# Optimization experiments

Measured on AMD Instinct MI355X. Metric: run time of the kernel, lower is better.

Reference implementation:

```python
import jax, jax.numpy as jnp
import numpy as np


def setup_inputs() -> dict:
    key = jax.random.key(0)
    k1, k2 = jax.random.split(key)
    B, C, H, W = 16, 8, 512, 512
    pred = jax.random.normal(k1, (B, C, H, W), dtype=jnp.float32)
    target = jax.random.randint(k2, (B, H, W), 0, C, dtype=jnp.int64)
    return {"pred": pred, "target": target}


def reference(pred, target):
    # pred: (B,C,H,W) float; target: (B,H,W) int64. reduction='mean', no weights.
    B, C, H, W = pred.shape

    # ---- J loss (vectorized over all (ci,ck) class pairs) ----
    t1h = jax.nn.one_hot(target, C, axis=1, dtype=pred.dtype)   # (B,C,H,W)
    n_i = t1h.sum(axis=(2, 3))                                   # (B,C) per-class pixel counts
    phi = t1h / n_i[:, :, None, None]                            # (B,C,H,W)
    # M[b,ci,ck] = sum_hw pred[b,ci]*phi[b,ck]
    M = jnp.einsum('bchw,bkhw->bck', pred, phi)
    diag = jnp.diagonal(M, axis1=1, axis2=2)                     # (B,C) = sum pred_ci*phi_ci
    # delta_ik contraction: sum pred_ci*(phi_ci - phi_ck)/2
    inner = (diag[:, :, None] - M) * 0.5                         # (B,C,C), zero on diagonal
    w = jnp.ones((C, C), dtype=pred.dtype)                       # default j_wgt
    off_diag = 1.0 - jnp.eye(C, dtype=pred.dtype)
    loss = w[None] * jnp.log(0.5 + inner) * off_diag[None]       # (B,C,C)
    j = -loss.sum(axis=(1, 2))                                   # (B,)
    jl = j.mean()

    # ---- cross entropy on collapsed dims: logits (B,C,N), target (B,N) ----
    logits = pred.reshape(B, C, H * W)
    logp = jax.nn.log_softmax(logits, axis=1)
    tgt = target.reshape(B, H * W)
    nll = -jnp.take_along_axis(logp, tgt[:, None, :], axis=1)[:, 0, :]  # (B,N)
    ce = nll.mean()

    return jl + ce
```

## Files before the change

### kernel.cpp

```cpp
#include <hip/hip_runtime.h>

#define NB 16
#define NC 8
#define HW (512 * 512)
#define BLOCKS_PER_B 32
#define NTHREADS 256

#define WS_FLOATS (NB * NC * NC + NB * NC + 1)

__device__ __forceinline__ float wave_reduce(float v) {
#pragma unroll
  for (int off = 32; off > 0; off >>= 1) v += __shfl_xor(v, off, 64);
  return v;
}

__global__ __launch_bounds__(NTHREADS, 2)
void jce_main(const float* __restrict__ pred, const int* __restrict__ target,
              float* __restrict__ ws) {
  const int b = blockIdx.y;
  const int tid = threadIdx.x;
  const float* predb = pred + (size_t)b * NC * HW;
  const int4* tgt4 = (const int4*)(target + (size_t)b * HW);

  float S[NC][NC];
  float cnt[NC];
  float ce = 0.0f;
#pragma unroll
  for (int i = 0; i < NC; ++i) {
    cnt[i] = 0.0f;
#pragma unroll
    for (int k = 0; k < NC; ++k) S[i][k] = 0.0f;
  }

  const int ng = HW / 4;
#pragma unroll 2
  for (int g = blockIdx.x * NTHREADS + tid; g < ng; g += BLOCKS_PER_B * NTHREADS) {
    const int4 t4 = tgt4[g];
    float4 p4[NC];
#pragma unroll
    for (int c = 0; c < NC; ++c)
      p4[c] = ((const float4*)(predb + (size_t)c * HW))[g];

#pragma unroll
    for (int j = 0; j < 4; ++j) {
      const int tc = (j == 0) ? t4.x : (j == 1) ? t4.y : (j == 2) ? t4.z : t4.w;
      float pv[NC];
#pragma unroll
      for (int c = 0; c < NC; ++c)
        pv[c] = (j == 0) ? p4[c].x : (j == 1) ? p4[c].y : (j == 2) ? p4[c].z : p4[c].w;

      float es = 0.0f;
#pragma unroll
      for (int c = 0; c < NC; ++c) es += __expf(pv[c]);
      const float lse = __logf(es);

      float ptc = 0.0f;
#pragma unroll
      for (int k = 0; k < NC; ++k) {
        const float msk = (tc == k) ? 1.0f : 0.0f;
        cnt[k] += msk;
        ptc = fmaf(msk, pv[k], ptc);
#pragma unroll
        for (int ci = 0; ci < NC; ++ci)
          S[ci][k] = fmaf(msk, pv[ci], S[ci][k]);
      }
      ce += lse - ptc;
    }
  }

#pragma unroll
  for (int i = 0; i < NC; ++i) {
#pragma unroll
    for (int k = 0; k < NC; ++k) S[i][k] = wave_reduce(S[i][k]);
    cnt[i] = wave_reduce(cnt[i]);
  }
  ce = wave_reduce(ce);

  __shared__ float red[NTHREADS / 64][NC * NC + NC + 1];
  const int wave = tid >> 6, lane = tid & 63;
  if (lane == 0) {
#pragma unroll
    for (int i = 0; i < NC; ++i) {
#pragma unroll
      for (int k = 0; k < NC; ++k) red[wave][i * NC + k] = S[i][k];
      red[wave][NC * NC + i] = cnt[i];
    }
    red[wave][NC * NC + NC] = ce;
  }
  __syncthreads();
  if (tid < NC * NC + NC + 1) {
    float v = 0.0f;
#pragma unroll
    for (int w = 0; w < NTHREADS / 64; ++w) v += red[w][tid];
    if (tid < NC * NC)
      atomicAdd(&ws[b * (NC * NC) + tid], v);
    else if (tid < NC * NC + NC)
      atomicAdd(&ws[NB * NC * NC + b * NC + (tid - NC * NC)], v);
    else
      atomicAdd(&ws[NB * NC * NC + NB * NC], v);
  }
}

__global__ __launch_bounds__(NTHREADS)
void jce_finalize(const float* __restrict__ ws, float* __restrict__ out) {
  const int tid = threadIdx.x;
  float acc = 0.0f;
  for (int idx = tid; idx < NB * NC * NC; idx += NTHREADS) {
    const int b = idx >> 6, ci = (idx >> 3) & 7, ck = idx & 7;
    if (ci == ck) continue;
    const float n_ck = ws[NB * NC * NC + b * NC + ck];
    const float n_ci = ws[NB * NC * NC + b * NC + ci];
    const float M = ws[b * (NC * NC) + ci * NC + ck] / n_ck;
    const float dg = ws[b * (NC * NC) + ci * NC + ci] / n_ci;
    acc += logf(0.5f + 0.5f * (dg - M));
  }
  acc = wave_reduce(acc);
  __shared__ float red[NTHREADS / 64];
  const int wave = tid >> 6, lane = tid & 63;
  if (lane == 0) red[wave] = acc;
  __syncthreads();
  if (tid == 0) {
    float tot = 0.0f;
#pragma unroll
    for (int w = 0; w < NTHREADS / 64; ++w) tot += red[w];
    const float jl = -tot / (float)NB;
    const float ce = ws[NB * NC * NC + NB * NC] / ((float)NB * (float)HW);
    out[0] = jl + ce;
  }
}

extern "C" void kernel_launch(void* const* d_in, const int* in_sizes, int n_in,
                              void* d_out, int out_size, void* d_ws, size_t ws_size,
                              hipStream_t stream) {
  const float* pred = (const float*)d_in[0];
  const int* target = (const int*)d_in[1];
  float* out = (float*)d_out;
  float* ws = (float*)d_ws;

  hipMemsetAsync(ws, 0, WS_FLOATS * sizeof(float), stream);
  dim3 grid(BLOCKS_PER_B, NB);
  jce_main<<<grid, NTHREADS, 0, stream>>>(pred, target, ws);
  jce_finalize<<<1, NTHREADS, 0, stream>>>(ws, out);
}
```

Baseline: 212.4 us.

## Software-pipeline loads with double buffers and fuse finalize via last-block counter

```diff
diff --git a/kernel.cpp b/kernel.cpp
--- a/kernel.cpp
+++ b/kernel.cpp
@@ -5,8 +5,11 @@
 #define HW (512 * 512)
 #define BLOCKS_PER_B 32
 #define NTHREADS 256
+#define NBLOCKS (BLOCKS_PER_B * NB)
+#define STRIDE (BLOCKS_PER_B * NTHREADS)
 
-#define WS_FLOATS (NB * NC * NC + NB * NC + 1)
+#define WS_FLOATS (NB * NC * NC + NB * NC + 2)
+#define CTR_IDX (NB * NC * NC + NB * NC + 1)
 
 __device__ __forceinline__ float wave_reduce(float v) {
 #pragma unroll
@@ -16,11 +19,12 @@
 
 __global__ __launch_bounds__(NTHREADS, 2)
 void jce_main(const float* __restrict__ pred, const int* __restrict__ target,
-              float* __restrict__ ws) {
+              float* __restrict__ ws, float* __restrict__ out) {
   const int b = blockIdx.y;
   const int tid = threadIdx.x;
   const float* predb = pred + (size_t)b * NC * HW;
   const int4* tgt4 = (const int4*)(target + (size_t)b * HW);
+  const int g0 = blockIdx.x * NTHREADS + tid;
 
   float S[NC][NC];
   float cnt[NC];
@@ -32,41 +36,50 @@
     for (int k = 0; k < NC; ++k) S[i][k] = 0.0f;
   }
 
-  const int ng = HW / 4;
-#pragma unroll 2
-  for (int g = blockIdx.x * NTHREADS + tid; g < ng; g += BLOCKS_PER_B * NTHREADS) {
-    const int4 t4 = tgt4[g];
-    float4 p4[NC];
+  int4 tA, tB;
+  float4 pA[NC], pB[NC];
+
+#define LOAD(T, P, s)                                                      \
+  do {                                                                     \
+    const int gg = g0 + (s) * STRIDE;                                      \
+    T = tgt4[gg];                                                          \
+    _Pragma("unroll") for (int c = 0; c < NC; ++c)                         \
+        P[c] = ((const float4*)(predb + (size_t)c * HW))[gg];              \
+  } while (0)
+
+#define COMPUTE(T, P)                                                      \
+  do {                                                                     \
+    _Pragma("unroll") for (int j = 0; j < 4; ++j) {                        \
+      const int tc = (j == 0) ? T.x : (j == 1) ? T.y : (j == 2) ? T.z : T.w; \
+      float pv[NC];                                                        \
+      _Pragma("unroll") for (int c = 0; c < NC; ++c)                       \
+          pv[c] = (j == 0) ? P[c].x : (j == 1) ? P[c].y                    \
+                  : (j == 2) ? P[c].z : P[c].w;                            \
+      float es = 0.0f;                                                     \
+      _Pragma("unroll") for (int c = 0; c < NC; ++c) es += __expf(pv[c]);  \
+      const float lse = __logf(es);                                        \
+      float ptc = 0.0f;                                                    \
+      _Pragma("unroll") for (int k = 0; k < NC; ++k) {                     \
+        const float msk = (tc == k) ? 1.0f : 0.0f;                         \
+        cnt[k] += msk;                                                     \
+        ptc = fmaf(msk, pv[k], ptc);                                       \
+        _Pragma("unroll") for (int ci = 0; ci < NC; ++ci)                  \
+            S[ci][k] = fmaf(msk, pv[ci], S[ci][k]);                        \
+      }                                                                    \
+      ce += lse - ptc;                                                     \
+    }                                                                      \
+  } while (0)
+
+  LOAD(tA, pA, 0);
 #pragma unroll
-    for (int c = 0; c < NC; ++c)
-      p4[c] = ((const float4*)(predb + (size_t)c * HW))[g];
-
-#pragma unroll
-    for (int j = 0; j < 4; ++j) {
-      const int tc = (j == 0) ? t4.x : (j == 1) ? t4.y : (j == 2) ? t4.z : t4.w;
-      float pv[NC];
-#pragma unroll
-      for (int c = 0; c < NC; ++c)
-        pv[c] = (j == 0) ? p4[c].x : (j == 1) ? p4[c].y : (j == 2) ? p4[c].z : p4[c].w;
-
-      float es = 0.0f;
-#pragma unroll
-      for (int c = 0; c < NC; ++c) es += __expf(pv[c]);
-      const float lse = __logf(es);
-
-      float ptc = 0.0f;
-#pragma unroll
-      for (int k = 0; k < NC; ++k) {
-        const float msk = (tc == k) ? 1.0f : 0.0f;
-        cnt[k] += msk;
-        ptc = fmaf(msk, pv[k], ptc);
-#pragma unroll
-        for (int ci = 0; ci < NC; ++ci)
-          S[ci][k] = fmaf(msk, pv[ci], S[ci][k]);
-      }
-      ce += lse - ptc;
-    }
+  for (int s = 0; s < 8; s += 2) {
+    if (s + 1 < 8) LOAD(tB, pB, s + 1);
+    COMPUTE(tA, pA);
+    if (s + 2 < 8) LOAD(tA, pA, s + 2);
+    if (s + 1 < 8) COMPUTE(tB, pB);
   }
+#undef LOAD
+#undef COMPUTE
 
 #pragma unroll
   for (int i = 0; i < NC; ++i) {
@@ -99,33 +112,38 @@
     else
       atomicAdd(&ws[NB * NC * NC + NB * NC], v);
   }
-}
 
-__global__ __launch_bounds__(NTHREADS)
-void jce_finalize(const float* __restrict__ ws, float* __restrict__ out) {
-  const int tid = threadIdx.x;
+  __shared__ int is_last;
+  __syncthreads();
+  if (tid == 0) {
+    __threadfence();
+    unsigned prev = atomicAdd((unsigned*)&ws[CTR_IDX], 1u);
+    is_last = (prev == (unsigned)(NBLOCKS - 1)) ? 1 : 0;
+  }
+  __syncthreads();
+  if (!is_last) return;
+
   float acc = 0.0f;
   for (int idx = tid; idx < NB * NC * NC; idx += NTHREADS) {
-    const int b = idx >> 6, ci = (idx >> 3) & 7, ck = idx & 7;
+    const int bb = idx >> 6, ci = (idx >> 3) & 7, ck = idx & 7;
     if (ci == ck) continue;
-    const float n_ck = ws[NB * NC * NC + b * NC + ck];
-    const float n_ci = ws[NB * NC * NC + b * NC + ci];
-    const float M = ws[b * (NC * NC) + ci * NC + ck] / n_ck;
-    const float dg = ws[b * (NC * NC) + ci * NC + ci] / n_ci;
-    acc += logf(0.5f + 0.5f * (dg - M));
+    const float n_ck = atomicAdd(&ws[NB * NC * NC + bb * NC + ck], 0.0f);
+    const float n_ci = atomicAdd(&ws[NB * NC * NC + bb * NC + ci], 0.0f);
+    const float Sik = atomicAdd(&ws[bb * (NC * NC) + ci * NC + ck], 0.0f);
+    const float Sii = atomicAdd(&ws[bb * (NC * NC) + ci * NC + ci], 0.0f);
+    acc += logf(0.5f + 0.5f * (Sii / n_ci - Sik / n_ck));
   }
   acc = wave_reduce(acc);
-  __shared__ float red[NTHREADS / 64];
-  const int wave = tid >> 6, lane = tid & 63;
-  if (lane == 0) red[wave] = acc;
+  __shared__ float red2[NTHREADS / 64];
+  if (lane == 0) red2[wave] = acc;
   __syncthreads();
   if (tid == 0) {
     float tot = 0.0f;
 #pragma unroll
-    for (int w = 0; w < NTHREADS / 64; ++w) tot += red[w];
+    for (int w = 0; w < NTHREADS / 64; ++w) tot += red2[w];
     const float jl = -tot / (float)NB;
-    const float ce = ws[NB * NC * NC + NB * NC] / ((float)NB * (float)HW);
-    out[0] = jl + ce;
+    const float cesum = atomicAdd(&ws[NB * NC * NC + NB * NC], 0.0f);
+    out[0] = jl + cesum / ((float)NB * (float)HW);
   }
 }
 
@@ -139,6 +157,5 @@
 
   hipMemsetAsync(ws, 0, WS_FLOATS * sizeof(float), stream);
   dim3 grid(BLOCKS_PER_B, NB);
-  jce_main<<<grid, NTHREADS, 0, stream>>>(pred, target, ws);
-  jce_finalize<<<1, NTHREADS, 0, stream>>>(ws, out);
+  jce_main<<<grid, NTHREADS, 0, stream>>>(pred, target, ws, out);
 }
```

Result: slower. 233.8 us (+10.1%).
